# Kernel optimization log

Measured on AMD Instinct MI355X. Metric: run time of the kernel, lower is better.

## Reference

```python
import jax, jax.numpy as jnp
import numpy as np


def _prelu(x, a):
    # nn.PReLU() with a single learnable parameter a
    return jnp.where(x >= 0, x, a * x)


def _conv1x1(x, w, b):
    # x: [n, cin, h, w], w: [cout, cin], b: [cout]
    return jnp.einsum('nchw,oc->nohw', x, w) + b[None, :, None, None]


def setup_inputs() -> dict:
    key = jax.random.key(0)
    ks = jax.random.split(key, 7)
    N, C, H, W = 8, 64, 64, 64
    red = 2
    c = C // red
    s = 1.0 / np.sqrt(C).astype(np.float32)
    x = jax.random.normal(ks[0], (N, C, H, W), dtype=jnp.float32)
    w1 = jax.random.normal(ks[1], (c, C), dtype=jnp.float32) * s
    b1 = jnp.zeros((c,), dtype=jnp.float32)
    w2 = jax.random.normal(ks[2], (c, C), dtype=jnp.float32) * s
    b2 = jnp.zeros((c,), dtype=jnp.float32)
    w3 = jax.random.normal(ks[3], (C, C), dtype=jnp.float32) * s
    b3 = jnp.zeros((C,), dtype=jnp.float32)
    a1 = jnp.full((1,), 0.25, dtype=jnp.float32)
    a2 = jnp.full((1,), 0.25, dtype=jnp.float32)
    a3 = jnp.full((1,), 0.25, dtype=jnp.float32)
    return {"x": x, "w1": w1, "b1": b1, "a1": a1, "w2": w2, "b2": b2,
            "a2": a2, "w3": w3, "b3": b3, "a3": a3}


def reference(x, w1, b1, a1, w2, b2, a2, w3, b3, a3):
    res_scale = 1.0
    n, C, h, w = x.shape
    e1 = _prelu(_conv1x1(x, w1, b1), a1[0])  # [n, c, h, w]
    e2 = _prelu(_conv1x1(x, w2, b2), a2[0])  # [n, c, h, w]
    e3 = _prelu(_conv1x1(x, w3, b3), a3[0])  # [n, C, h, w]
    c = e1.shape[1]
    hw = h * w
    q = e1.transpose(0, 2, 3, 1).reshape(n, hw, c)   # [n, hw, c]
    k = e2.reshape(n, c, hw)                         # [n, c, hw]
    score = jax.nn.softmax(jnp.matmul(q, k), axis=-1)  # [n, hw, hw]
    v = e3.reshape(n, C, hw).transpose(0, 2, 1)      # [n, hw, C]
    out = jnp.matmul(score, v)                       # [n, hw, C]
    out = out.transpose(0, 2, 1).reshape(n, C, h, w)
    return out + res_scale * x
```

## Files before the change

### kernel.cpp

```cpp
#include <hip/hip_runtime.h>
#include <hip/hip_bf16.h>

typedef __bf16 bf16x8 __attribute__((ext_vector_type(8)));
typedef __bf16 bf16x4 __attribute__((ext_vector_type(4)));
typedef float  f32x4  __attribute__((ext_vector_type(4)));

#define SEQ 4096
#define CIN 64
#define KBLK 128
#define NT (SEQ / KBLK)
#define LOG2E 1.44269504088896340736f

__device__ __forceinline__ void gll16(const void* g, void* l) {
    __builtin_amdgcn_global_load_lds(
        (const __attribute__((address_space(1))) void*)g,
        (__attribute__((address_space(3))) void*)l, 16, 0, 0);
}

__global__ __launch_bounds__(256, 2) void qkv_gen(
    const float* __restrict__ x,
    const float* __restrict__ w1, const float* __restrict__ b1, const float* __restrict__ a1,
    const float* __restrict__ w2, const float* __restrict__ b2, const float* __restrict__ a2,
    const float* __restrict__ w3, const float* __restrict__ b3, const float* __restrict__ a3,
    __bf16* __restrict__ qws, __bf16* __restrict__ kws, __bf16* __restrict__ vtws)
{
    __shared__ float xs[CIN][64];
    __shared__ float wl[CIN][128];
    __shared__ float bl[128];
    __shared__ float al[4];

    const int t  = threadIdx.x;
    const int n  = blockIdx.x >> 6;
    const int p0 = (blockIdx.x & 63) << 6;

    for (int idx = t; idx < 2048; idx += 256) {
        int j = idx >> 6, c = idx & 63;
        wl[c][j]      = w1[idx];
        wl[c][32 + j] = w2[idx];
    }
    for (int idx = t; idx < 4096; idx += 256) {
        int j = idx >> 6, c = idx & 63;
        wl[c][64 + j] = w3[idx];
    }
    if (t < 32) { bl[t] = b1[t]; bl[32 + t] = b2[t]; }
    if (t >= 128 && t < 192) bl[64 + (t - 128)] = b3[t - 128];
    if (t == 0) { al[0] = a1[0]; al[1] = a2[0]; al[2] = a3[0]; }

    const float* xb = x + ((size_t)n * CIN) * SEQ + p0;
    for (int r = 0; r < 16; ++r) {
        int e = r * 256 + t;
        xs[e >> 6][e & 63] = xb[(size_t)(e >> 6) * SEQ + (e & 63)];
    }
    __syncthreads();

    const int p  = t & 63;
    const int g  = t >> 6;
    const int jb = g << 5;
    const float a = (g == 0) ? al[0] : ((g == 1) ? al[1] : al[2]);

    float acc[32];
    #pragma unroll
    for (int j = 0; j < 32; ++j) acc[j] = bl[jb + j];

    for (int c = 0; c < CIN; ++c) {
        float xv = xs[c][p];
        const f32x4* wr = (const f32x4*)&wl[c][jb];
        #pragma unroll
        for (int j4 = 0; j4 < 8; ++j4) {
            f32x4 wv = wr[j4];
            acc[j4*4+0] = fmaf(wv[0], xv, acc[j4*4+0]);
            acc[j4*4+1] = fmaf(wv[1], xv, acc[j4*4+1]);
            acc[j4*4+2] = fmaf(wv[2], xv, acc[j4*4+2]);
            acc[j4*4+3] = fmaf(wv[3], xv, acc[j4*4+3]);
        }
    }
    #pragma unroll
    for (int j = 0; j < 32; ++j) acc[j] = acc[j] >= 0.f ? acc[j] : a * acc[j];

    const int pg = p0 + p;
    if (g <= 1) {
        const float sc = (g == 0) ? LOG2E : 1.0f;
        __bf16* dst = (g == 0 ? qws : kws) + ((size_t)n * SEQ + pg) * 32;
        #pragma unroll
        for (int v8 = 0; v8 < 4; ++v8) {
            bf16x8 o;
            #pragma unroll
            for (int i = 0; i < 8; ++i) o[i] = (__bf16)(acc[v8*8+i] * sc);
            *(bf16x8*)(dst + v8*8) = o;
        }
    } else {
        __bf16* dst = vtws + ((size_t)n * CIN + (jb - 64)) * SEQ + pg;
        #pragma unroll
        for (int j = 0; j < 32; ++j) dst[(size_t)j * SEQ] = (__bf16)acc[j];
    }
}

__global__ __launch_bounds__(256, 2) void attn(
    const __bf16* __restrict__ qws, const __bf16* __restrict__ kws,
    const __bf16* __restrict__ vtws, const float* __restrict__ x,
    float* __restrict__ out)
{
    __shared__ __align__(16) char kt[2][KBLK * 64];
    __shared__ __align__(16) char vt[2][CIN * 256];
    __shared__ __align__(16) char pt[4][16 * 256];

    const int t    = threadIdx.x;
    const int lane = t & 63;
    const int wid  = t >> 6;
    const int n    = blockIdx.x & 7;
    const int qblk = blockIdx.x >> 3;
    const int r16  = lane & 15;
    const int g4   = lane >> 4;
    const int qbase = qblk * 64 + wid * 16;
    const int sw   = (r16 & 7) << 4;

    const char* kb = (const char*)(kws + (size_t)n * SEQ * 32);
    const char* vb = (const char*)(vtws + (size_t)n * CIN * SEQ);
    char* pw = &pt[wid][0];

    const bf16x8 qf = *(const bf16x8*)((const char*)(qws + (size_t)n * SEQ * 32)
                                       + (size_t)(qbase + r16) * 64 + g4 * 16);

    f32x4 of[4] = {};
    f32x4 ll4 = {0.f, 0.f, 0.f, 0.f};

    auto stage = [&](int k0n, int buf) {
        const char* ks = kb + (size_t)k0n * 64;
        #pragma unroll
        for (int j = 0; j < 2; ++j) {
            int off = wid * 2048 + j * 1024;
            gll16(ks + off + lane * 16, &kt[buf][0] + off);
        }
        #pragma unroll
        for (int j = 0; j < 4; ++j) {
            int L    = wid * 4096 + j * 1024;
            int row  = (L >> 8) + (lane >> 4);
            int colb = (lane & 15) * 16;
            const char* vs = vb + (size_t)row * 8192 + k0n * 2 + (colb ^ ((row & 7) << 4));
            gll16(vs, &vt[buf][0] + L);
        }
    };

    stage(0, 0);
    __syncthreads();

    for (int tt = 0; tt < NT; ++tt) {
        const int cur = tt & 1;
        if (tt + 1 < NT) stage((tt + 1) * KBLK, cur ^ 1);

        const char* kc_ = &kt[cur][0];
        const char* vc_ = &vt[cur][0];

        f32x4 st[8];
        __builtin_amdgcn_s_setprio(1);
        #pragma unroll
        for (int f = 0; f < 8; ++f) {
            bf16x8 kf = *(const bf16x8*)(kc_ + (f * 16 + r16) * 64 + g4 * 16);
            f32x4 z = {0.f, 0.f, 0.f, 0.f};
            st[f] = __builtin_amdgcn_mfma_f32_16x16x32_bf16(kf, qf, z, 0, 0, 0);
        }
        __builtin_amdgcn_s_setprio(0);

        #pragma unroll
        for (int f = 0; f < 8; ++f) {
            f32x4 e;
            e[0] = __builtin_exp2f(st[f][0]);
            e[1] = __builtin_exp2f(st[f][1]);
            e[2] = __builtin_exp2f(st[f][2]);
            e[3] = __builtin_exp2f(st[f][3]);
            ll4 += e;
            bf16x4 pk;
            pk[0] = (__bf16)e[0]; pk[1] = (__bf16)e[1];
            pk[2] = (__bf16)e[2]; pk[3] = (__bf16)e[3];
            *(bf16x4*)(pw + r16 * 256 + ((f * 32 + g4 * 8) ^ sw)) = pk;
        }

        __builtin_amdgcn_s_setprio(1);
        #pragma unroll
        for (int kc2 = 0; kc2 < 4; ++kc2) {
            bf16x8 pf = *(const bf16x8*)(pw + r16 * 256 + ((kc2 * 64 + g4 * 16) ^ sw));
            #pragma unroll
            for (int fd = 0; fd < 4; ++fd) {
                bf16x8 vf = *(const bf16x8*)(vc_ + (fd * 16 + r16) * 256
                                             + ((kc2 * 64 + g4 * 16) ^ sw));
                of[fd] = __builtin_amdgcn_mfma_f32_16x16x32_bf16(vf, pf, of[fd], 0, 0, 0);
            }
        }
        __builtin_amdgcn_s_setprio(0);

        __syncthreads();
    }

    float llr = ll4[0] + ll4[1] + ll4[2] + ll4[3];
    llr += __shfl_xor(llr, 16);
    llr += __shfl_xor(llr, 32);
    const float inv = 1.f / llr;
    const int qg = qbase + r16;
    const float* xb = x + (size_t)n * CIN * SEQ;
    float* ob = out + (size_t)n * CIN * SEQ;
    #pragma unroll
    for (int fd = 0; fd < 4; ++fd)
        #pragma unroll
        for (int r = 0; r < 4; ++r) {
            size_t idx = (size_t)(fd * 16 + g4 * 4 + r) * SEQ + qg;
            ob[idx] = of[fd][r] * inv + xb[idx];
        }
}

extern "C" void kernel_launch(void* const* d_in, const int* in_sizes, int n_in,
                              void* d_out, int out_size, void* d_ws, size_t ws_size,
                              hipStream_t stream)
{
    (void)in_sizes; (void)n_in; (void)out_size; (void)ws_size;
    const float* x  = (const float*)d_in[0];
    const float* w1 = (const float*)d_in[1];
    const float* b1 = (const float*)d_in[2];
    const float* a1 = (const float*)d_in[3];
    const float* w2 = (const float*)d_in[4];
    const float* b2 = (const float*)d_in[5];
    const float* a2 = (const float*)d_in[6];
    const float* w3 = (const float*)d_in[7];
    const float* b3 = (const float*)d_in[8];
    const float* a3 = (const float*)d_in[9];
    float* out = (float*)d_out;

    __bf16* qws  = (__bf16*)d_ws;
    __bf16* kws  = qws + (size_t)8 * SEQ * 32;
    __bf16* vtws = kws + (size_t)8 * SEQ * 32;

    hipLaunchKernelGGL(qkv_gen, dim3(512), dim3(256), 0, stream,
                       x, w1, b1, a1, w2, b2, a2, w3, b3, a3, qws, kws, vtws);
    hipLaunchKernelGGL(attn, dim3(512), dim3(256), 0, stream,
                       qws, kws, vtws, x, out);
}
```

Baseline: 84.78 us.

## Process two 16-row query tiles per wave to reuse K/V fragments

The attention kernel now runs two waves per block instead of four, and each wave handles 32 query rows, keeping two sets of accumulators. Each K and V fragment read from LDS feeds two MFMAs, which halves LDS traffic per FLOP. The K tile in LDS also gets an XOR swizzle to cut bank conflicts. The cost is higher register pressure, no min-blocks occupancy hint, and fewer waves per block to hide latency.

Result: slower. 105.1 us (+24.0%).

```diff
diff --git a/kernel.cpp b/kernel.cpp
--- a/kernel.cpp
+++ b/kernel.cpp
@@ -95,14 +95,14 @@
     }
 }
 
-__global__ __launch_bounds__(256, 2) void attn(
+__global__ __launch_bounds__(128) void attn(
     const __bf16* __restrict__ qws, const __bf16* __restrict__ kws,
     const __bf16* __restrict__ vtws, const float* __restrict__ x,
     float* __restrict__ out)
 {
     __shared__ __align__(16) char kt[2][KBLK * 64];
     __shared__ __align__(16) char vt[2][CIN * 256];
-    __shared__ __align__(16) char pt[4][16 * 256];
+    __shared__ __align__(16) char pt[2][32 * 256];
 
     const int t    = threadIdx.x;
     const int lane = t & 63;
@@ -111,33 +111,36 @@
     const int qblk = blockIdx.x >> 3;
     const int r16  = lane & 15;
     const int g4   = lane >> 4;
-    const int qbase = qblk * 64 + wid * 16;
+    const int qbase = qblk * 64 + wid * 32;
     const int sw   = (r16 & 7) << 4;
+    const int ksw  = ((r16 >> 1) & 3) << 4;
 
     const char* kb = (const char*)(kws + (size_t)n * SEQ * 32);
     const char* vb = (const char*)(vtws + (size_t)n * CIN * SEQ);
     char* pw = &pt[wid][0];
 
-    const bf16x8 qf = *(const bf16x8*)((const char*)(qws + (size_t)n * SEQ * 32)
-                                       + (size_t)(qbase + r16) * 64 + g4 * 16);
-
-    f32x4 of[4] = {};
-    f32x4 ll4 = {0.f, 0.f, 0.f, 0.f};
+    const char* qbase_p = (const char*)(qws + (size_t)n * SEQ * 32);
+    const bf16x8 qf0 = *(const bf16x8*)(qbase_p + (size_t)(qbase + r16) * 64 + g4 * 16);
+    const bf16x8 qf1 = *(const bf16x8*)(qbase_p + (size_t)(qbase + 16 + r16) * 64 + g4 * 16);
+
+    f32x4 of0[4] = {}, of1[4] = {};
+    f32x4 ls0 = {0.f,0.f,0.f,0.f}, ls1 = {0.f,0.f,0.f,0.f};
 
     auto stage = [&](int k0n, int buf) {
-        const char* ks = kb + (size_t)k0n * 64;
-        #pragma unroll
-        for (int j = 0; j < 2; ++j) {
-            int off = wid * 2048 + j * 1024;
-            gll16(ks + off + lane * 16, &kt[buf][0] + off);
-        }
         #pragma unroll
         for (int j = 0; j < 4; ++j) {
-            int L    = wid * 4096 + j * 1024;
-            int row  = (L >> 8) + (lane >> 4);
-            int colb = (lane & 15) * 16;
-            const char* vs = vb + (size_t)row * 8192 + k0n * 2 + (colb ^ ((row & 7) << 4));
-            gll16(vs, &vt[buf][0] + L);
+            int L   = j * 2048 + t * 16;
+            int row = L >> 6;
+            int c16 = (t & 3) ^ ((t >> 3) & 3);
+            gll16(kb + (size_t)(k0n + row) * 64 + c16 * 16, &kt[buf][0] + L);
+        }
+        #pragma unroll
+        for (int j = 0; j < 8; ++j) {
+            int L    = j * 2048 + t * 16;
+            int row  = L >> 8;
+            int colb = (t & 15) * 16;
+            gll16(vb + (size_t)row * 8192 + k0n * 2 + (colb ^ ((row & 7) << 4)),
+                  &vt[buf][0] + L);
         }
     };
 
@@ -151,39 +154,55 @@
         const char* kc_ = &kt[cur][0];
         const char* vc_ = &vt[cur][0];
 
-        f32x4 st[8];
+        f32x4 st0[8], st1[8];
         __builtin_amdgcn_s_setprio(1);
         #pragma unroll
         for (int f = 0; f < 8; ++f) {
-            bf16x8 kf = *(const bf16x8*)(kc_ + (f * 16 + r16) * 64 + g4 * 16);
+            bf16x8 kf = *(const bf16x8*)(kc_ + (f * 16 + r16) * 64 + (g4 * 16 ^ ksw));
             f32x4 z = {0.f, 0.f, 0.f, 0.f};
-            st[f] = __builtin_amdgcn_mfma_f32_16x16x32_bf16(kf, qf, z, 0, 0, 0);
+            st0[f] = __builtin_amdgcn_mfma_f32_16x16x32_bf16(kf, qf0, z, 0, 0, 0);
+            st1[f] = __builtin_amdgcn_mfma_f32_16x16x32_bf16(kf, qf1, z, 0, 0, 0);
         }
         __builtin_amdgcn_s_setprio(0);
 
         #pragma unroll
         for (int f = 0; f < 8; ++f) {
             f32x4 e;
-            e[0] = __builtin_exp2f(st[f][0]);
-            e[1] = __builtin_exp2f(st[f][1]);
-            e[2] = __builtin_exp2f(st[f][2]);
-            e[3] = __builtin_exp2f(st[f][3]);
-            ll4 += e;
+            e[0] = __builtin_exp2f(st0[f][0]);
+            e[1] = __builtin_exp2f(st0[f][1]);
+            e[2] = __builtin_exp2f(st0[f][2]);
+            e[3] = __builtin_exp2f(st0[f][3]);
+            ls0 += e;
             bf16x4 pk;
             pk[0] = (__bf16)e[0]; pk[1] = (__bf16)e[1];
             pk[2] = (__bf16)e[2]; pk[3] = (__bf16)e[3];
             *(bf16x4*)(pw + r16 * 256 + ((f * 32 + g4 * 8) ^ sw)) = pk;
         }
+        #pragma unroll
+        for (int f = 0; f < 8; ++f) {
+            f32x4 e;
+            e[0] = __builtin_exp2f(st1[f][0]);
+            e[1] = __builtin_exp2f(st1[f][1]);
+            e[2] = __builtin_exp2f(st1[f][2]);
+            e[3] = __builtin_exp2f(st1[f][3]);
+            ls1 += e;
+            bf16x4 pk;
+            pk[0] = (__bf16)e[0]; pk[1] = (__bf16)e[1];
+            pk[2] = (__bf16)e[2]; pk[3] = (__bf16)e[3];
+            *(bf16x4*)(pw + (16 + r16) * 256 + ((f * 32 + g4 * 8) ^ sw)) = pk;
+        }
 
         __builtin_amdgcn_s_setprio(1);
         #pragma unroll
         for (int kc2 = 0; kc2 < 4; ++kc2) {
-            bf16x8 pf = *(const bf16x8*)(pw + r16 * 256 + ((kc2 * 64 + g4 * 16) ^ sw));
+            const int col = (kc2 * 64 + g4 * 16) ^ sw;
+            bf16x8 pf0 = *(const bf16x8*)(pw + r16 * 256 + col);
+            bf16x8 pf1 = *(const bf16x8*)(pw + (16 + r16) * 256 + col);
             #pragma unroll
             for (int fd = 0; fd < 4; ++fd) {
-                bf16x8 vf = *(const bf16x8*)(vc_ + (fd * 16 + r16) * 256
-                                             + ((kc2 * 64 + g4 * 16) ^ sw));
-                of[fd] = __builtin_amdgcn_mfma_f32_16x16x32_bf16(vf, pf, of[fd], 0, 0, 0);
+                bf16x8 vf = *(const bf16x8*)(vc_ + (fd * 16 + r16) * 256 + col);
+                of0[fd] = __builtin_amdgcn_mfma_f32_16x16x32_bf16(vf, pf0, of0[fd], 0, 0, 0);
+                of1[fd] = __builtin_amdgcn_mfma_f32_16x16x32_bf16(vf, pf1, of1[fd], 0, 0, 0);
             }
         }
         __builtin_amdgcn_s_setprio(0);
@@ -191,19 +210,20 @@
         __syncthreads();
     }
 
-    float llr = ll4[0] + ll4[1] + ll4[2] + ll4[3];
-    llr += __shfl_xor(llr, 16);
-    llr += __shfl_xor(llr, 32);
-    const float inv = 1.f / llr;
-    const int qg = qbase + r16;
+    float l0 = ls0[0] + ls0[1] + ls0[2] + ls0[3];
+    float l1 = ls1[0] + ls1[1] + ls1[2] + ls1[3];
+    l0 += __shfl_xor(l0, 16); l0 += __shfl_xor(l0, 32);
+    l1 += __shfl_xor(l1, 16); l1 += __shfl_xor(l1, 32);
+    const float inv0 = 1.f / l0, inv1 = 1.f / l1;
     const float* xb = x + (size_t)n * CIN * SEQ;
     float* ob = out + (size_t)n * CIN * SEQ;
     #pragma unroll
     for (int fd = 0; fd < 4; ++fd)
         #pragma unroll
         for (int r = 0; r < 4; ++r) {
-            size_t idx = (size_t)(fd * 16 + g4 * 4 + r) * SEQ + qg;
-            ob[idx] = of[fd][r] * inv + xb[idx];
+            size_t rowoff = (size_t)(fd * 16 + g4 * 4 + r) * SEQ + qbase + r16;
+            ob[rowoff]      = of0[fd][r] * inv0 + xb[rowoff];
+            ob[rowoff + 16] = of1[fd][r] * inv1 + xb[rowoff + 16];
         }
 }
 
@@ -230,6 +250,6 @@
 
     hipLaunchKernelGGL(qkv_gen, dim3(512), dim3(256), 0, stream,
                        x, w1, b1, a1, w2, b2, a2, w3, b3, a3, qws, kws, vtws);
-    hipLaunchKernelGGL(attn, dim3(512), dim3(256), 0, stream,
+    hipLaunchKernelGGL(attn, dim3(512), dim3(128), 0, stream,
                        qws, kws, vtws, x, out);
 }
```

## Switch attention to 32x32 MFMA with register-resident P via permlane swap

Applied to the files above, without the earlier changes.

The attention kernel moves from 16x16x32 to 32x32x16 bf16 MFMA tiles, with each wave handling 32 queries and blocks shrunk to 2 waves. The probability tile is packed with v_cvt_pk_bf16_f32 and rearranged across lanes with v_permlane32_swap, so it stays in registers instead of going through an LDS round trip. The key block drops to 64 and the K/V LDS swizzles change to match the new fragment layout. This removes LDS writes and reads for P and doubles work per MFMA, but adds a barrier per smaller tile and fewer waves per block.

New measurement: 129.5 us. 1.53x slower.

```diff
diff --git a/kernel.cpp b/kernel.cpp
--- a/kernel.cpp
+++ b/kernel.cpp
@@ -2,12 +2,13 @@
 #include <hip/hip_bf16.h>
 
 typedef __bf16 bf16x8 __attribute__((ext_vector_type(8)));
-typedef __bf16 bf16x4 __attribute__((ext_vector_type(4)));
 typedef float  f32x4  __attribute__((ext_vector_type(4)));
+typedef float  f32x16 __attribute__((ext_vector_type(16)));
+typedef int    i32x4  __attribute__((ext_vector_type(4)));
 
 #define SEQ 4096
 #define CIN 64
-#define KBLK 128
+#define KBLK 64
 #define NT (SEQ / KBLK)
 #define LOG2E 1.44269504088896340736f
 
@@ -15,6 +16,12 @@
     __builtin_amdgcn_global_load_lds(
         (const __attribute__((address_space(1))) void*)g,
         (__attribute__((address_space(3))) void*)l, 16, 0, 0);
+}
+
+__device__ __forceinline__ unsigned cvtpk(float lo, float hi) {
+    unsigned r;
+    asm("v_cvt_pk_bf16_f32 %0, %1, %2" : "=v"(r) : "v"(lo), "v"(hi));
+    return r;
 }
 
 __global__ __launch_bounds__(256, 2) void qkv_gen(
@@ -95,49 +102,50 @@
     }
 }
 
-__global__ __launch_bounds__(256, 2) void attn(
+__global__ __launch_bounds__(128) void attn(
     const __bf16* __restrict__ qws, const __bf16* __restrict__ kws,
     const __bf16* __restrict__ vtws, const float* __restrict__ x,
     float* __restrict__ out)
 {
-    __shared__ __align__(16) char kt[2][KBLK * 64];
-    __shared__ __align__(16) char vt[2][CIN * 256];
-    __shared__ __align__(16) char pt[4][16 * 256];
+    __shared__ __align__(16) char ktl[2][KBLK * 64];
+    __shared__ __align__(16) char vtl[2][CIN * KBLK*2];
 
     const int t    = threadIdx.x;
     const int lane = t & 63;
     const int wid  = t >> 6;
     const int n    = blockIdx.x & 7;
     const int qblk = blockIdx.x >> 3;
-    const int r16  = lane & 15;
-    const int g4   = lane >> 4;
-    const int qbase = qblk * 64 + wid * 16;
-    const int sw   = (r16 & 7) << 4;
+    const int l31  = lane & 31;
+    const int h    = lane >> 5;
+    const int qbase = qblk * 64 + wid * 32;
+    const int ksw  = ((l31 >> 1) & 3) << 4;
+    const int vsw  = (l31 & 7) << 4;
 
     const char* kb = (const char*)(kws + (size_t)n * SEQ * 32);
     const char* vb = (const char*)(vtws + (size_t)n * CIN * SEQ);
-    char* pw = &pt[wid][0];
-
-    const bf16x8 qf = *(const bf16x8*)((const char*)(qws + (size_t)n * SEQ * 32)
-                                       + (size_t)(qbase + r16) * 64 + g4 * 16);
-
-    f32x4 of[4] = {};
-    f32x4 ll4 = {0.f, 0.f, 0.f, 0.f};
+
+    const char* qp = (const char*)(qws + (size_t)n * SEQ * 32)
+                     + (size_t)(qbase + l31) * 64 + h * 16;
+    const bf16x8 qf0 = *(const bf16x8*)(qp);
+    const bf16x8 qf1 = *(const bf16x8*)(qp + 32);
+
+    f32x16 of0 = {}, of1 = {};
+    float ls = 0.f;
 
     auto stage = [&](int k0n, int buf) {
-        const char* ks = kb + (size_t)k0n * 64;
         #pragma unroll
         for (int j = 0; j < 2; ++j) {
-            int off = wid * 2048 + j * 1024;
-            gll16(ks + off + lane * 16, &kt[buf][0] + off);
+            int L   = j * 2048 + t * 16;
+            int row = L >> 6;
+            int c16 = (t & 3) ^ ((t >> 3) & 3);
+            gll16(kb + (size_t)(k0n + row) * 64 + c16 * 16, &ktl[buf][0] + L);
         }
         #pragma unroll
         for (int j = 0; j < 4; ++j) {
-            int L    = wid * 4096 + j * 1024;
-            int row  = (L >> 8) + (lane >> 4);
-            int colb = (lane & 15) * 16;
-            const char* vs = vb + (size_t)row * 8192 + k0n * 2 + (colb ^ ((row & 7) << 4));
-            gll16(vs, &vt[buf][0] + L);
+            int L    = j * 2048 + t * 16;
+            int row  = L >> 7;
+            int colb = ((t & 7) ^ ((t >> 3) & 7)) << 4;
+            gll16(vb + (size_t)row * 8192 + (size_t)k0n * 2 + colb, &vtl[buf][0] + L);
         }
     };
 
@@ -148,63 +156,71 @@
         const int cur = tt & 1;
         if (tt + 1 < NT) stage((tt + 1) * KBLK, cur ^ 1);
 
-        const char* kc_ = &kt[cur][0];
-        const char* vc_ = &vt[cur][0];
-
-        f32x4 st[8];
+        const char* kc_ = &ktl[cur][0];
+        const char* vc_ = &vtl[cur][0];
+
+        unsigned c0[8], c1[8];
+
+        #pragma unroll
+        for (int kti = 0; kti < 2; ++kti) {
+            const char* krow = kc_ + (size_t)(kti * 32 + l31) * 64;
+            bf16x8 kf0 = *(const bf16x8*)(krow + ((h * 16) ^ ksw));
+            bf16x8 kf1 = *(const bf16x8*)(krow + ((32 + h * 16) ^ ksw));
+            f32x16 s = {};
+            __builtin_amdgcn_s_setprio(1);
+            s = __builtin_amdgcn_mfma_f32_32x32x16_bf16(kf0, qf0, s, 0, 0, 0);
+            s = __builtin_amdgcn_mfma_f32_32x32x16_bf16(kf1, qf1, s, 0, 0, 0);
+            __builtin_amdgcn_s_setprio(0);
+
+            float p[16];
+            #pragma unroll
+            for (int r = 0; r < 16; ++r) {
+                p[r] = __builtin_exp2f(s[r]);
+                ls += p[r];
+            }
+            unsigned* c = kti ? c1 : c0;
+            #pragma unroll
+            for (int j = 0; j < 4; ++j) {
+                c[j]     = cvtpk(p[2*j],     p[2*j + 1]);
+                c[4 + j] = cvtpk(p[8 + 2*j], p[9 + 2*j]);
+            }
+            asm("v_permlane32_swap_b32 %0, %1" : "+v"(c[0]), "+v"(c[2]));
+            asm("v_permlane32_swap_b32 %0, %1" : "+v"(c[1]), "+v"(c[3]));
+            asm("v_permlane32_swap_b32 %0, %1" : "+v"(c[4]), "+v"(c[6]));
+            asm("v_permlane32_swap_b32 %0, %1" : "+v"(c[5]), "+v"(c[7]));
+        }
+
         __builtin_amdgcn_s_setprio(1);
         #pragma unroll
-        for (int f = 0; f < 8; ++f) {
-            bf16x8 kf = *(const bf16x8*)(kc_ + (f * 16 + r16) * 64 + g4 * 16);
-            f32x4 z = {0.f, 0.f, 0.f, 0.f};
-            st[f] = __builtin_amdgcn_mfma_f32_16x16x32_bf16(kf, qf, z, 0, 0, 0);
+        for (int s4 = 0; s4 < 4; ++s4) {
+            const unsigned* cs = (s4 < 2) ? c0 : c1;
+            const int sl = (s4 & 1) * 4;
+            i32x4 bi = { (int)cs[sl], (int)cs[sl+1], (int)cs[sl+2], (int)cs[sl+3] };
+            bf16x8 pf = __builtin_bit_cast(bf16x8, bi);
+            const int colv = (s4 * 32 + h * 16) ^ vsw;
+            bf16x8 vf0 = *(const bf16x8*)(vc_ + (size_t)l31 * 128 + colv);
+            bf16x8 vf1 = *(const bf16x8*)(vc_ + (size_t)(32 + l31) * 128 + colv);
+            of0 = __builtin_amdgcn_mfma_f32_32x32x16_bf16(vf0, pf, of0, 0, 0, 0);
+            of1 = __builtin_amdgcn_mfma_f32_32x32x16_bf16(vf1, pf, of1, 0, 0, 0);
         }
         __builtin_amdgcn_s_setprio(0);
 
-        #pragma unroll
-        for (int f = 0; f < 8; ++f) {
-            f32x4 e;
-            e[0] = __builtin_exp2f(st[f][0]);
-            e[1] = __builtin_exp2f(st[f][1]);
-            e[2] = __builtin_exp2f(st[f][2]);
-            e[3] = __builtin_exp2f(st[f][3]);
-            ll4 += e;
-            bf16x4 pk;
-            pk[0] = (__bf16)e[0]; pk[1] = (__bf16)e[1];
-            pk[2] = (__bf16)e[2]; pk[3] = (__bf16)e[3];
-            *(bf16x4*)(pw + r16 * 256 + ((f * 32 + g4 * 8) ^ sw)) = pk;
-        }
-
-        __builtin_amdgcn_s_setprio(1);
-        #pragma unroll
-        for (int kc2 = 0; kc2 < 4; ++kc2) {
-            bf16x8 pf = *(const bf16x8*)(pw + r16 * 256 + ((kc2 * 64 + g4 * 16) ^ sw));
-            #pragma unroll
-            for (int fd = 0; fd < 4; ++fd) {
-                bf16x8 vf = *(const bf16x8*)(vc_ + (fd * 16 + r16) * 256
-                                             + ((kc2 * 64 + g4 * 16) ^ sw));
-                of[fd] = __builtin_amdgcn_mfma_f32_16x16x32_bf16(vf, pf, of[fd], 0, 0, 0);
-            }
-        }
-        __builtin_amdgcn_s_setprio(0);
-
         __syncthreads();
     }
 
-    float llr = ll4[0] + ll4[1] + ll4[2] + ll4[3];
-    llr += __shfl_xor(llr, 16);
-    llr += __shfl_xor(llr, 32);
-    const float inv = 1.f / llr;
-    const int qg = qbase + r16;
+    float ll = ls + __shfl_xor(ls, 32);
+    const float inv = 1.f / ll;
+    const int qg = qbase + l31;
     const float* xb = x + (size_t)n * CIN * SEQ;
     float* ob = out + (size_t)n * CIN * SEQ;
     #pragma unroll
-    for (int fd = 0; fd < 4; ++fd)
-        #pragma unroll
-        for (int r = 0; r < 4; ++r) {
-            size_t idx = (size_t)(fd * 16 + g4 * 4 + r) * SEQ + qg;
-            ob[idx] = of[fd][r] * inv + xb[idx];
-        }
+    for (int r = 0; r < 16; ++r) {
+        int dv = (r & 3) + 8 * (r >> 2) + 4 * h;
+        size_t i0 = (size_t)dv * SEQ + qg;
+        size_t i1 = (size_t)(dv + 32) * SEQ + qg;
+        ob[i0] = of0[r] * inv + xb[i0];
+        ob[i1] = of1[r] * inv + xb[i1];
+    }
 }
 
 extern "C" void kernel_launch(void* const* d_in, const int* in_sizes, int n_in,
@@ -230,6 +246,6 @@
 
     hipLaunchKernelGGL(qkv_gen, dim3(512), dim3(256), 0, stream,
                        x, w1, b1, a1, w2, b2, a2, w3, b3, a3, qws, kws, vtws);
-    hipLaunchKernelGGL(attn, dim3(512), dim3(256), 0, stream,
+    hipLaunchKernelGGL(attn, dim3(512), dim3(128), 0, stream,
                        qws, kws, vtws, x, out);
 }
```
